# Performance work log

Measured on AMD Instinct MI355X. Metric: run time of the kernel, lower is better.

## Reference

```python
import jax, jax.numpy as jnp
import numpy as np

EPS = 1e-5

def mvn(x):
    # per-(N,C) spatial mean/std normalization; torch .var is unbiased (ddof=1)
    mean = jnp.mean(x, axis=(2, 3), keepdims=True)
    var = jnp.var(x, axis=(2, 3), ddof=1, keepdims=True)
    return (x - mean) / jnp.sqrt(var + EPS)

def conv1x1(x, w, b):
    # w: [O, C] (1x1 conv collapsed), x: [B, C, H, W]
    return jnp.einsum('bchw,oc->bohw', x, w) + b[None, :, None, None]

def conv3x3(x, w, b):
    # w: [O, I, 3, 3], VALID padding (snet uses padding=0)
    y = jax.lax.conv_general_dilated(x, w, (1, 1), 'VALID',
                                     dimension_numbers=('NCHW', 'OIHW', 'NCHW'))
    return y + b[None, :, None, None]

def safe_cbrt(x):
    # pow(relu(x), 1/3) with safe gradient at 0 (forward identical)
    pos = x > 0
    return jnp.where(pos, jnp.power(jnp.where(pos, x, 1.0), 1.0 / 3.0), 0.0)

def _forward(content, style, wf_san, bf_san, wg_san, bg_san, wh_san, bh_san,
             wf_mcc, bf_mcc, wg_mcc, bg_mcc, w_fc, b_fc, w_out, b_out,
             wc1, bc1, wc2, bc2, wc3, bc3, ws1, bs1, ws2, bs2, ws3, bs3,
             w_unc, b_unc):
    B, C, H, W = content.shape
    cn = mvn(content)
    sn = mvn(style)

    # --- MCC branch: channel correlation statistic of style ---
    F_Fc = conv1x1(cn, wf_mcc, bf_mcc)                      # [B,C,H,W]
    g = conv1x1(sn, wg_mcc, bg_mcc).reshape(B, C, H * W)    # [B,C,HW]
    FC_S = jnp.sum(g * g, axis=-1) / jnp.sum(g, axis=-1)    # [B,C]
    FC_S = FC_S @ w_fc.T + b_fc                             # Linear
    part1 = F_Fc * FC_S[:, :, None, None]

    # --- WCT-like covariance branch (compressed 32-dim space) ---
    Fs0 = style - jnp.mean(style, axis=(2, 3), keepdims=True)  # nor_mean
    fc_ = conv1x1(jax.nn.relu(conv1x1(jax.nn.relu(conv1x1(cn, wc1, bc1)), wc2, bc2)), wc3, bc3)  # [B,32,H,W]
    fs_ = conv1x1(jax.nn.relu(conv3x3(jax.nn.relu(conv3x3(Fs0, ws1, bs1)), ws2, bs2)), ws3, bs3)  # [B,32,H-4,W-4]
    cdim = fc_.shape[1]
    fs_flat = fs_.reshape(B, cdim, -1)                       # [B,32,hw_s]
    cov = jnp.einsum('bci,bdi->bcd', fs_flat, fs_flat) / fs_flat.shape[2]  # [B,32,32]
    out = jnp.einsum('bcd,bdi->bci', cov, fc_.reshape(B, cdim, H * W)).reshape(B, cdim, H, W)
    part2 = conv1x1(out, w_unc, b_unc)                       # [B,512,H,W]

    # --- SANet-style attention branch ---
    F_s = conv1x1(cn, wf_san, bf_san).reshape(B, C, H * W)
    G_s = conv1x1(sn, wg_san, bg_san).reshape(B, C, H * W)
    H_s = conv1x1(style, wh_san, bh_san).reshape(B, C, H * W)
    S = jax.nn.softmax(jnp.einsum('bci,bcj->bij', F_s, G_s), axis=-1)  # [B,HW,HW]
    part3 = jnp.einsum('bcj,bij->bci', H_s, S).reshape(B, C, H, W)

    p = safe_cbrt(jax.nn.relu(part1 * part2 * part3))
    return conv1x1(p, w_out, b_out) + content


def setup_inputs() -> dict:
    key = jax.random.key(0)
    B, C, H, W = 16, 512, 32, 32
    s = 0.02
    shapes = {
        'content': (B, C, H, W), 'style': (B, C, H, W),
        'wf_san': (C, C), 'bf_san': (C,), 'wg_san': (C, C), 'bg_san': (C,),
        'wh_san': (C, C), 'bh_san': (C,),
        'wf_mcc': (C, C), 'bf_mcc': (C,), 'wg_mcc': (C, C), 'bg_mcc': (C,),
        'w_fc': (C, C), 'b_fc': (C,), 'w_out': (C, C), 'b_out': (C,),
        'wc1': (256, 512), 'bc1': (256,), 'wc2': (128, 256), 'bc2': (128,),
        'wc3': (32, 128), 'bc3': (32,),
        'ws1': (256, 512, 3, 3), 'bs1': (256,), 'ws2': (128, 256, 3, 3), 'bs2': (128,),
        'ws3': (32, 128), 'bs3': (32,),
        'w_unc': (512, 32), 'b_unc': (512,),
    }
    d = {}
    for i, (name, shp) in enumerate(shapes.items()):
        k = jax.random.fold_in(key, i)
        scale = 1.0 if name in ('content', 'style') else s
        d[name] = jax.random.normal(k, shp, dtype=jnp.float32) * scale
    return d


def reference(content, style, wf_san, bf_san, wg_san, bg_san, wh_san, bh_san,
              wf_mcc, bf_mcc, wg_mcc, bg_mcc, w_fc, b_fc, w_out, b_out,
              wc1, bc1, wc2, bc2, wc3, bc3, ws1, bs1, ws2, bs2, ws3, bs3,
              w_unc, b_unc):
    return _forward(content, style, wf_san, bf_san, wg_san, bg_san, wh_san, bh_san,
                    wf_mcc, bf_mcc, wg_mcc, bg_mcc, w_fc, b_fc, w_out, b_out,
                    wc1, bc1, wc2, bc2, wc3, bc3, ws1, bs1, ws2, bs2, ws3, bs3,
                    w_unc, b_unc)
```

## Files before the change

### kernel.cpp

```cpp
#include <hip/hip_runtime.h>
#include <hip/hip_bf16.h>
#include <hip/hip_fp16.h>
#include <math.h>


typedef __attribute__((ext_vector_type(8))) short short8;
typedef __attribute__((ext_vector_type(4))) float f32x4;
typedef unsigned short us;
#define MFMA16 __builtin_amdgcn_mfma_f32_16x16x32_bf16

struct h16 { us v; };

template <class A, class B> struct SameT { static constexpr bool v = false; };
template <class A> struct SameT<A, A> { static constexpr bool v = true; };

__device__ inline float b2f(us b) { return __uint_as_float(((unsigned)b) << 16); }
__device__ inline us f2b(float f) {
    unsigned u = __float_as_uint(f);
    return (us)((u + 0x7FFFu + ((u >> 16) & 1u)) >> 16);
}

template <typename TOUT>
__device__ inline us cvt2b(float x) {
    if constexpr (SameT<TOUT, h16>::v) return __half_as_ushort(__float2half(x));
    else return f2b(x);
}

__device__ inline double blockReduceSumD(double v, double* sh) {
    int t = threadIdx.x;
    sh[t] = v; __syncthreads();
    for (int s = blockDim.x >> 1; s > 0; s >>= 1) {
        if (t < s) sh[t] += sh[t + s];
        __syncthreads();
    }
    double r = sh[0]; __syncthreads();
    return r;
}

__global__ __launch_bounds__(256) void stats_k(const float* __restrict__ X,
                                               float* __restrict__ mean,
                                               float* __restrict__ inv, int HW) {
    __shared__ double sh[256];
    int bc = blockIdx.x;
    const float* x = X + (size_t)bc * HW;
    int t = threadIdx.x;
    float v[4];
    double s = 0.0;
    #pragma unroll
    for (int r = 0; r < 4; ++r) { v[r] = x[t + r * 256]; s += (double)v[r]; }
    double tot = blockReduceSumD(s, sh);
    double ss = 0.0;
    #pragma unroll
    for (int r = 0; r < 4; ++r) ss += (double)v[r] * (double)v[r];
    double tot2 = blockReduceSumD(ss, sh);
    if (t == 0) {
        double m = tot / HW;
        double var = (tot2 - tot * tot / HW) / (HW - 1);
        mean[bc] = (float)m;
        inv[bc] = (float)(1.0 / sqrt(var + 1e-5));
    }
}

__global__ __launch_bounds__(256) void trn_k(const float* __restrict__ X,
                                             const float* __restrict__ mean,
                                             const float* __restrict__ inv,
                                             us* __restrict__ Yn, us* __restrict__ Yc,
                                             us* __restrict__ Yr, int C, int HW) {
    __shared__ us Ln[64 * 65];
    __shared__ us Lc[64 * 65];
    __shared__ us Lr[64 * 65];
    int bz = blockIdx.z, c0 = blockIdx.y * 64, h0 = blockIdx.x * 64;
    const float* Xb = X + (size_t)bz * C * HW;
    int t = threadIdx.x;
    int cl = t >> 3, h8 = (t & 7) * 8;
    #pragma unroll
    for (int half = 0; half < 2; ++half) {
        int c = cl + half * 32;
        int gc = c0 + c;
        float m = mean[bz * C + gc], iv = inv[bz * C + gc];
        const float4* s4 = (const float4*)&Xb[(size_t)gc * HW + h0 + h8];
        float4 f0 = s4[0], f1 = s4[1];
        float vv[8] = {f0.x, f0.y, f0.z, f0.w, f1.x, f1.y, f1.z, f1.w};
        #pragma unroll
        for (int i = 0; i < 8; ++i) {
            int li = c * 65 + h8 + i;
            if (Yn) Ln[li] = f2b((vv[i] - m) * iv);
            if (Yc) Lc[li] = f2b(vv[i] - m);
            if (Yr) Lr[li] = f2b(vv[i]);
        }
    }
    __syncthreads();
    int hl = t >> 3, c8 = (t & 7) * 8;
    #pragma unroll
    for (int half = 0; half < 2; ++half) {
        int hh = hl + half * 32;
        size_t off = ((size_t)bz * HW + h0 + hh) * (size_t)C + c0 + c8;
        us tmp[8];
        if (Yn) {
            #pragma unroll
            for (int i = 0; i < 8; ++i) tmp[i] = Ln[(c8 + i) * 65 + hh];
            *(uint4*)&Yn[off] = *(const uint4*)tmp;
        }
        if (Yc) {
            #pragma unroll
            for (int i = 0; i < 8; ++i) tmp[i] = Lc[(c8 + i) * 65 + hh];
            *(uint4*)&Yc[off] = *(const uint4*)tmp;
        }
        if (Yr) {
            #pragma unroll
            for (int i = 0; i < 8; ++i) tmp[i] = Lr[(c8 + i) * 65 + hh];
            *(uint4*)&Yr[off] = *(const uint4*)tmp;
        }
    }
}

template <typename TE>
__device__ inline void stage16(const TE* __restrict__ src, bool valid, us* dst) {
    us tmp[16];
    if (valid) {
        if constexpr (sizeof(TE) == 2) {
            uint4 a = ((const uint4*)src)[0], b = ((const uint4*)src)[1];
            *(uint4*)&tmp[0] = a; *(uint4*)&tmp[8] = b;
        } else {
            const float4* s4 = (const float4*)src;
            float4 f0 = s4[0], f1 = s4[1], f2 = s4[2], f3 = s4[3];
            float vv[16] = {f0.x, f0.y, f0.z, f0.w, f1.x, f1.y, f1.z, f1.w,
                            f2.x, f2.y, f2.z, f2.w, f3.x, f3.y, f3.z, f3.w};
            #pragma unroll
            for (int i = 0; i < 16; ++i) tmp[i] = f2b(vv[i]);
        }
    } else {
        #pragma unroll
        for (int i = 0; i < 16; ++i) tmp[i] = 0;
    }
    ((uint4*)dst)[0] = *(uint4*)&tmp[0];
    ((uint4*)dst)[1] = *(uint4*)&tmp[8];
}

template <typename TAel, typename TBel, typename TOUT, int OUTT>
__global__ __launch_bounds__(256) void mf2_k(const TAel* __restrict__ A, long astride, int lda,
                                             const TBel* __restrict__ B, long bstride, int ldb,
                                             const float* __restrict__ bias,
                                             TOUT* __restrict__ Y,
                                             const float* __restrict__ add_src,
                                             int K, int M, int N, int relu) {
    __shared__ __align__(16) us smem[20480];
    int bz = blockIdx.z;
    int mbase = blockIdx.y * 128, nbase = blockIdx.x * 128;
    const TAel* Ab = A + (size_t)bz * astride;
    const TBel* Bb = B + (size_t)bz * bstride;
    int t = threadIdx.x;
    int row = t & 127, kh = t >> 7;
    int wave = t >> 6, lane = t & 63, lm = lane & 15, q = lane >> 4;
    int mh = (wave >> 1) * 64, nh = (wave & 1) * 64;
    int gm = mbase + row, gn = nbase + row;
    bool vm = gm < M, vn = gn < N;

    auto As = [&](int buf) { return smem + buf * 5120; };
    auto Bs = [&](int buf) { return smem + 10240 + buf * 5120; };

    auto stage = [&](int buf, int kb) {
        stage16(Ab + (size_t)gm * lda + kb + kh * 16, vm, As(buf) + row * 40 + kh * 16);
        stage16(Bb + (size_t)gn * ldb + kb + kh * 16, vn, Bs(buf) + row * 40 + kh * 16);
    };

    f32x4 acc[4][4];
    #pragma unroll
    for (int i = 0; i < 4; ++i)
        #pragma unroll
        for (int j = 0; j < 4; ++j) acc[i][j] = (f32x4){0.f, 0.f, 0.f, 0.f};

    stage(0, 0);
    __syncthreads();
    int cur = 0;
    for (int kb = 0; kb < K; kb += 32) {
        if (kb + 32 < K) stage(cur ^ 1, kb + 32);
        short8 af[4], bf[4];
        #pragma unroll
        for (int i = 0; i < 4; ++i) af[i] = *(const short8*)(As(cur) + (mh + i * 16 + lm) * 40 + q * 8);
        #pragma unroll
        for (int j = 0; j < 4; ++j) bf[j] = *(const short8*)(Bs(cur) + (nh + j * 16 + lm) * 40 + q * 8);
        #pragma unroll
        for (int i = 0; i < 4; ++i)
            #pragma unroll
            for (int j = 0; j < 4; ++j)
                acc[i][j] = MFMA16(af[i], bf[j], acc[i][j], 0, 0, 0);
        __syncthreads();
        cur ^= 1;
    }

    if constexpr (sizeof(TOUT) == 2) {
        if (mbase + 128 <= M && nbase + 128 <= N) {
            us* Ts = smem;
            #pragma unroll
            for (int i = 0; i < 4; ++i) {
                int m0 = mh + i * 16 + q * 4;
                float bv[4];
                #pragma unroll
                for (int r = 0; r < 4; ++r) bv[r] = bias ? bias[mbase + m0 + r] : 0.f;
                #pragma unroll
                for (int j = 0; j < 4; ++j) {
                    int nl = nh + j * 16 + lm;
                    #pragma unroll
                    for (int r = 0; r < 4; ++r) {
                        float x = acc[i][j][r] + bv[r];
                        if (relu) x = (x > 0.f) ? x : 0.f;
                        us val = cvt2b<TOUT>(x);
                        if (OUTT == 0) Ts[(m0 + r) * 136 + nl] = val;
                        else Ts[nl * 136 + m0 + r] = val;
                    }
                }
            }
            __syncthreads();
            #pragma unroll
            for (int k2 = 0; k2 < 8; ++k2) {
                int flat = k2 * 256 + t;
                int r0 = flat >> 4, u = flat & 15;
                uint4 vv = *(const uint4*)&Ts[r0 * 136 + u * 8];
                us* dst;
                if (OUTT == 0)
                    dst = (us*)&Y[((size_t)bz * M + mbase + r0) * N + nbase + u * 8];
                else
                    dst = (us*)&Y[((size_t)bz * N + nbase + r0) * M + mbase + u * 8];
                *(uint4*)dst = vv;
            }
            return;
        }
    }

    #pragma unroll
    for (int i = 0; i < 4; ++i) {
        int m0 = mbase + mh + i * 16 + q * 4;
        if (m0 >= M) continue;
        float bv[4];
        #pragma unroll
        for (int r = 0; r < 4; ++r) bv[r] = bias ? bias[m0 + r] : 0.f;
        #pragma unroll
        for (int j = 0; j < 4; ++j) {
            int n = nbase + nh + j * 16 + lm;
            if (n >= N) continue;
            float v[4];
            #pragma unroll
            for (int r = 0; r < 4; ++r) {
                float x = acc[i][j][r] + bv[r];
                if (relu) x = (x > 0.f) ? x : 0.f;
                v[r] = x;
            }
            if (OUTT == 1) {
                size_t off = ((size_t)bz * N + n) * (size_t)M + m0;
                if constexpr (sizeof(TOUT) == 2) {
                    us o4[4];
                    #pragma unroll
                    for (int r = 0; r < 4; ++r) o4[r] = cvt2b<TOUT>(v[r]);
                    *(uint2*)&Y[off] = *(const uint2*)o4;
                } else {
                    float4 f4 = make_float4(v[0], v[1], v[2], v[3]);
                    *(float4*)&Y[off] = f4;
                }
            } else {
                #pragma unroll
                for (int r = 0; r < 4; ++r) {
                    size_t off = ((size_t)bz * M + m0 + r) * (size_t)N + n;
                    float x = v[r];
                    if (add_src) x += add_src[off];
                    if constexpr (sizeof(TOUT) == 2) {
                        us val = cvt2b<TOUT>(x);
                        *(us*)&Y[off] = val;
                    } else Y[off] = x;
                }
            }
        }
    }
}

struct SBias {
    const float* bp[10];
    int moff[10];
    unsigned relu;
};

__global__ __launch_bounds__(256) void reorder_gw_k(const us* __restrict__ W,
                                                    us* __restrict__ Wf, int M, int K) {
    int idx = blockIdx.x * 256 + threadIdx.x;
    int KB = K >> 5;
    int total = (M >> 7) * KB * 8 * 64;
    if (idx >= total) return;
    int lane = idx & 63;
    int f = idx >> 6;
    int i = f & 3, mhalf = (f >> 2) & 1;
    int rest = f >> 3;
    int kb = rest % KB, mt = rest / KB;
    int row = mt * 128 + mhalf * 64 + i * 16 + (lane & 15);
    int col = kb * 32 + (lane >> 4) * 8;
    *(uint4*)&Wf[(size_t)idx * 8] = *(const uint4*)&W[(size_t)row * K + col];
}

template <typename TBel, typename TOUT, int OUTT>
__global__ __launch_bounds__(256) void mfw_k(const us* __restrict__ Wf,
                                             const TBel* __restrict__ B, long bstride, int ldb,
                                             TOUT* __restrict__ Y, int ldy,
                                             SBias sb, const float* __restrict__ add_src,
                                             int K, int M, int N) {
    __shared__ __align__(16) us smem[10240];
    int bz = blockIdx.z, mt = blockIdx.y;
    int mbase = mt * 128, nbase = blockIdx.x * 128;
    const TBel* Bb = B + (size_t)bz * bstride;
    int t = threadIdx.x;
    int row = t & 127, kh = t >> 7;
    int wave = t >> 6, lane = t & 63, lm = lane & 15, q = lane >> 4;
    int mhalf = wave >> 1, nh = (wave & 1) * 64;
    int KB = K >> 5;
    const us* Wb = Wf + (size_t)mt * KB * 4096;
    int relu = (sb.relu >> mt) & 1;
    const float* bias = sb.bp[mt];
    int moff = sb.moff[mt];

    auto Bs = [&](int buf) { return smem + buf * 5120; };
    auto stageB = [&](int buf, int kb) {
        stage16(Bb + (size_t)(nbase + row) * ldb + (size_t)kb * 32 + kh * 16, true,
                Bs(buf) + row * 40 + kh * 16);
    };

    f32x4 acc[4][4];
    #pragma unroll
    for (int i = 0; i < 4; ++i)
        #pragma unroll
        for (int j = 0; j < 4; ++j) acc[i][j] = (f32x4){0.f, 0.f, 0.f, 0.f};

    stageB(0, 0);
    __syncthreads();
    int cur = 0;
    for (int kb = 0; kb < KB; ++kb) {
        if (kb + 1 < KB) stageB(cur ^ 1, kb + 1);
        const us* wk = Wb + (size_t)kb * 4096 + mhalf * 2048;
        short8 af[4], bf[4];
        #pragma unroll
        for (int i = 0; i < 4; ++i) af[i] = *(const short8*)&wk[i * 512 + lane * 8];
        #pragma unroll
        for (int j = 0; j < 4; ++j) bf[j] = *(const short8*)(Bs(cur) + (nh + j * 16 + lm) * 40 + q * 8);
        #pragma unroll
        for (int i = 0; i < 4; ++i)
            #pragma unroll
            for (int j = 0; j < 4; ++j)
                acc[i][j] = MFMA16(af[i], bf[j], acc[i][j], 0, 0, 0);
        __syncthreads();
        cur ^= 1;
    }

    if constexpr (sizeof(TOUT) == 2) {
        us* Ts = smem;
        #pragma unroll
        for (int p = 0; p < 2; ++p) {
            bool part = (OUTT == 1) ? ((wave & 1) == p) : (mhalf == p);
            if (part) {
                #pragma unroll
                for (int i = 0; i < 4; ++i) {
                    int m0 = mhalf * 64 + i * 16 + q * 4;
                    float bv[4];
                    #pragma unroll
                    for (int r = 0; r < 4; ++r) bv[r] = bias[mbase + m0 + r - moff];
                    #pragma unroll
                    for (int j = 0; j < 4; ++j) {
                        int nl = nh + j * 16 + lm;
                        #pragma unroll
                        for (int r = 0; r < 4; ++r) {
                            float x = acc[i][j][r] + bv[r];
                            if (relu) x = (x > 0.f) ? x : 0.f;
                            us val = cvt2b<TOUT>(x);
                            if (OUTT == 1) Ts[(nl - p * 64) * 136 + m0 + r] = val;
                            else Ts[(m0 + r - p * 64) * 136 + nl] = val;
                        }
                    }
                }
            }
            __syncthreads();
            #pragma unroll
            for (int k2 = 0; k2 < 4; ++k2) {
                int flat = k2 * 256 + t;
                int r0 = flat >> 4, u = flat & 15;
                uint4 vv = *(const uint4*)&Ts[r0 * 136 + u * 8];
                us* dst;
                if (OUTT == 1)
                    dst = (us*)&Y[((size_t)bz * N + nbase + p * 64 + r0) * ldy + mbase + u * 8];
                else
                    dst = (us*)&Y[((size_t)bz * M + mbase + p * 64 + r0) * (size_t)N + nbase + u * 8];
                *(uint4*)dst = vv;
            }
            __syncthreads();
        }
    } else {
        #pragma unroll
        for (int i = 0; i < 4; ++i) {
            int m0 = mbase + mhalf * 64 + i * 16 + q * 4;
            float bv[4];
            #pragma unroll
            for (int r = 0; r < 4; ++r) bv[r] = bias[m0 + r - moff];
            #pragma unroll
            for (int j = 0; j < 4; ++j) {
                int n = nbase + nh + j * 16 + lm;
                #pragma unroll
                for (int r = 0; r < 4; ++r) {
                    size_t off = ((size_t)bz * M + m0 + r) * (size_t)N + n;
                    float x = acc[i][j][r] + bv[r];
                    if (relu) x = (x > 0.f) ? x : 0.f;
                    if (add_src) x += add_src[off];
                    Y[off] = x;
                }
            }
        }
    }
}

struct CpyArg {
    const float* src[11];
    unsigned long long dstoff[11];
    int len[11];
};
__global__ __launch_bounds__(256) void wcat_k(CpyArg a, us* __restrict__ arena) {
    int seg = blockIdx.y;
    int idx = blockIdx.x * 256 + threadIdx.x;
    if (idx < a.len[seg]) arena[a.dstoff[seg] + idx] = f2b(a.src[seg][idx]);
}

__global__ __launch_bounds__(256) void reorder_wf_k(const float* __restrict__ W,
                                                    us* __restrict__ Wf, int O, int Cin) {
    int idx = blockIdx.x * 256 + threadIdx.x;
    int OT = O >> 6, KB = Cin >> 5;
    int total = OT * KB * 9 * 4 * 64;
    if (idx >= total) return;
    int lane = idx & 63;
    int f = idx >> 6;
    int i = f & 1, half = (f >> 1) & 1;
    int tf = f >> 2;
    int tap = tf % 9;
    int rest = tf / 9;
    int kb = rest % KB, ot = rest / KB;
    int o = ot * 64 + half * 32 + i * 16 + (lane & 15);
    int cb = kb * 32 + (lane >> 4) * 8;
    us v[8];
    #pragma unroll
    for (int e = 0; e < 8; ++e)
        v[e] = f2b(W[((size_t)o * Cin + cb + e) * 9 + tap]);
    *(uint4*)&Wf[(size_t)idx * 8] = *(const uint4*)v;
}

template <int PR>
__device__ inline void stage_patch(const us* __restrict__ Xb, us* __restrict__ dst,
                                   int pyb, int kb, int Cin, int IH, int IW, int t) {
    const int ITEMS = (2 * PR + 2) * 36 * 4;
    for (int i = t; i < ITEMS; i += 256) {
        int p = i >> 2, q8 = (i & 3) * 8;
        int r = p / 36, x = p - r * 36;
        int gy = pyb + r;
        uint4 v = make_uint4(0u, 0u, 0u, 0u);
        if (x < IW && gy < IH)
            v = *(const uint4*)&Xb[((size_t)(gy * IW + x)) * Cin + kb * 32 + q8];
        *(uint4*)&dst[p * 40 + q8] = v;
    }
}

template <int PR>
__global__ __launch_bounds__(256) void conv_mf4_k(const us* __restrict__ X, long xbstride,
                                                  const us* __restrict__ Wf,
                                                  const float* __restrict__ bias,
                                                  us* __restrict__ Y, long ybstride,
                                                  int Cin, int O, int IH, int IW,
                                                  int OH, int OW) {
    __shared__ us patch[2][(2 * PR + 2) * 36 * 40];
    int bz = blockIdx.z;
    int obase = blockIdx.y * 64;
    int pyb = blockIdx.x * (2 * PR);
    const us* Xb = X + (size_t)bz * xbstride;
    int t = threadIdx.x;
    int wave = t >> 6, lane = t & 63, lm = lane & 15, q = lane >> 4;
    int half = wave >> 1, rw = wave & 1;
    int KB = Cin >> 5;
    const us* Wb = Wf + (size_t)(obase >> 6) * KB * 9 * 2048;

    f32x4 acc[PR][2][2];
    #pragma unroll
    for (int pr = 0; pr < PR; ++pr)
        #pragma unroll
        for (int i = 0; i < 2; ++i)
            #pragma unroll
            for (int j = 0; j < 2; ++j) acc[pr][i][j] = (f32x4){0.f, 0.f, 0.f, 0.f};

    stage_patch<PR>(Xb, patch[0], pyb, 0, Cin, IH, IW, t);
    __syncthreads();
    int cur = 0;
    for (int kb = 0; kb < KB; ++kb) {
        if (kb + 1 < KB) stage_patch<PR>(Xb, patch[cur ^ 1], pyb, kb + 1, Cin, IH, IW, t);
        const us* Wk = Wb + (size_t)kb * 9 * 2048;
        #pragma unroll
        for (int tap = 0; tap < 9; ++tap) {
            int ky = tap / 3, kx = tap - ky * 3;
            const us* wt = Wk + tap * 2048 + half * 1024;
            short8 a0 = *(const short8*)&wt[lane * 8];
            short8 a1 = *(const short8*)&wt[512 + lane * 8];
            #pragma unroll
            for (int pr = 0; pr < PR; ++pr) {
                int prow = (pr * 2 + rw + ky) * 36;
                short8 b0 = *(const short8*)&patch[cur][(prow + lm + kx) * 40 + q * 8];
                short8 b1 = *(const short8*)&patch[cur][(prow + 16 + lm + kx) * 40 + q * 8];
                acc[pr][0][0] = MFMA16(a0, b0, acc[pr][0][0], 0, 0, 0);
                acc[pr][0][1] = MFMA16(a0, b1, acc[pr][0][1], 0, 0, 0);
                acc[pr][1][0] = MFMA16(a1, b0, acc[pr][1][0], 0, 0, 0);
                acc[pr][1][1] = MFMA16(a1, b1, acc[pr][1][1], 0, 0, 0);
            }
        }
        __syncthreads();
        cur ^= 1;
    }

    us* Yb = Y + (size_t)bz * ybstride;
    #pragma unroll
    for (int pr = 0; pr < PR; ++pr) {
        int py = pyb + pr * 2 + rw;
        if (py >= OH) continue;
        #pragma unroll
        for (int i = 0; i < 2; ++i) {
            int m0 = obase + half * 32 + i * 16 + q * 4;
            #pragma unroll
            for (int j = 0; j < 2; ++j) {
                int px = j * 16 + lm;
                if (px >= OW) continue;
                us o4[4];
                #pragma unroll
                for (int r = 0; r < 4; ++r) {
                    float v = acc[pr][i][j][r] + bias[m0 + r];
                    v = (v > 0.f) ? v : 0.f;
                    o4[r] = f2b(v);
                }
                *(uint2*)&Yb[((size_t)(py * OW + px)) * O + m0] = *(const uint2*)o4;
            }
        }
    }
}

__global__ __launch_bounds__(256) void gemm_k(const float* __restrict__ W,
                                              const float* __restrict__ X,
                                              const float* __restrict__ bias,
                                              float* __restrict__ Y,
                                              int C, int O, int N) {
    int obase = blockIdx.y * 32;
    __shared__ float As[32][33];
    __shared__ float Bs[32][33];
    int t = threadIdx.x;
    int tx = t & 15, ty = t >> 4;
    float acc00 = 0, acc01 = 0, acc10 = 0, acc11 = 0;
    for (int cb = 0; cb < C; cb += 32) {
        int k = t & 31, o0 = t >> 5;
        #pragma unroll
        for (int r = 0; r < 4; ++r) {
            int ol = o0 + r * 8;
            As[k][ol] = W[(size_t)(obase + ol) * C + cb + k];
        }
        int n0 = t & 31, k0 = t >> 5;
        #pragma unroll
        for (int r = 0; r < 4; ++r) {
            int k2 = k0 + r * 8;
            Bs[k2][n0] = (n0 < N) ? X[(size_t)(cb + k2) * N + n0] : 0.f;
        }
        __syncthreads();
        #pragma unroll
        for (int k2 = 0; k2 < 32; ++k2) {
            float a0 = As[k2][ty], a1 = As[k2][ty + 16];
            float b0 = Bs[k2][tx], b1 = Bs[k2][tx + 16];
            acc00 += a0 * b0; acc01 += a0 * b1;
            acc10 += a1 * b0; acc11 += a1 * b1;
        }
        __syncthreads();
    }
    float accs[2][2] = {{acc00, acc01}, {acc10, acc11}};
    #pragma unroll
    for (int i = 0; i < 2; ++i) {
        int o = obase + ty + i * 16;
        float bv = bias[o];
        #pragma unroll
        for (int j = 0; j < 2; ++j) {
            int n = tx + j * 16;
            if (n < N) Y[(size_t)o * N + n] = accs[i][j] + bv;
        }
    }
}

__global__ __launch_bounds__(256) void fcs3a_k(const us* __restrict__ g, int ldg,
                                               float* __restrict__ pa, int HW) {
    int b = blockIdx.x, j = blockIdx.y;
    int t = threadIdx.x;
    const us* gb = g + ((size_t)b * HW + (size_t)j * 128) * ldg + 2 * t;
    double s0 = 0.0, s1 = 0.0;
    #pragma unroll 4
    for (int hw = 0; hw < 128; ++hw) {
        unsigned u = *(const unsigned*)&gb[(size_t)hw * ldg];
        float f0 = b2f((us)(u & 0xFFFFu));
        float f1 = b2f((us)(u >> 16));
        s0 += (double)f0 * (double)f0;
        s1 += (double)f1 * (double)f1;
    }
    float2 w = make_float2((float)s0, (float)s1);
    *(float2*)&pa[((size_t)b * 8 + j) * 512 + 2 * t] = w;
}

__global__ __launch_bounds__(256) void fcs3b_k(const float* __restrict__ pa,
                                               const float* __restrict__ bg,
                                               float* __restrict__ fcs, int B, int HW) {
    int b = blockIdx.x;
    int t = threadIdx.x;
    double s0 = 0.0, s1 = 0.0;
    #pragma unroll
    for (int j = 0; j < 8; ++j) {
        float2 w = *(const float2*)&pa[((size_t)b * 8 + j) * 512 + 2 * t];
        s0 += (double)w.x; s1 += (double)w.y;
    }
    int c0 = 2 * t;
    fcs[(size_t)c0 * B + b] = (float)(s0 / ((double)HW * (double)bg[c0]));
    fcs[(size_t)(c0 + 1) * B + b] = (float)(s1 / ((double)HW * (double)bg[c0 + 1]));
}

__global__ __launch_bounds__(256) void softmax_k(const us* __restrict__ S,
                                                 us* __restrict__ P) {
    __shared__ float sh[256];
    size_t row = blockIdx.x;
    const us* r = S + row * 1024;
    us* po = P + row * 1024;
    int t = threadIdx.x;
    us raw[4];
    *(uint2*)raw = *(const uint2*)&r[t * 4];
    float v[4];
    float m = -INFINITY;
    #pragma unroll
    for (int i = 0; i < 4; ++i) {
        v[i] = __half2float(__ushort_as_half(raw[i]));
        m = fmaxf(m, v[i]);
    }
    sh[t] = m; __syncthreads();
    for (int s = 128; s > 0; s >>= 1) { if (t < s) sh[t] = fmaxf(sh[t], sh[t + s]); __syncthreads(); }
    m = sh[0]; __syncthreads();
    float sum = 0;
    #pragma unroll
    for (int i = 0; i < 4; ++i) { v[i] = expf(v[i] - m); sum += v[i]; }
    sh[t] = sum; __syncthreads();
    for (int s = 128; s > 0; s >>= 1) { if (t < s) sh[t] += sh[t + s]; __syncthreads(); }
    float inv = 1.f / sh[0]; __syncthreads();
    #pragma unroll
    for (int i = 0; i < 4; ++i) raw[i] = f2b(v[i] * inv);
    *(uint2*)&po[t * 4] = *(const uint2*)raw;
}

__global__ __launch_bounds__(256) void cov2_k(const float* __restrict__ fs,
                                              float* __restrict__ cov, int Cd, int M) {
    __shared__ float Ls[196 * 36];
    int bb = blockIdx.x;
    int t = threadIdx.x;
    const float* p = fs + (size_t)bb * M * Cd;
    int c = t >> 3, d0 = (t & 7) * 4;
    float a0 = 0.f, a1 = 0.f, a2 = 0.f, a3 = 0.f;
    for (int ch = 0; ch < 4; ++ch) {
        __syncthreads();
        for (int i = t; i < 1568; i += 256) {
            int rowi = i >> 3, c4 = (i & 7) * 4;
            float4 v = *(const float4*)&p[(size_t)(ch * 196 + rowi) * Cd + c4];
            *(float4*)&Ls[rowi * 36 + c4] = v;
        }
        __syncthreads();
        for (int i = 0; i < 196; ++i) {
            float a = Ls[i * 36 + c];
            a0 += a * Ls[i * 36 + d0 + 0];
            a1 += a * Ls[i * 36 + d0 + 1];
            a2 += a * Ls[i * 36 + d0 + 2];
            a3 += a * Ls[i * 36 + d0 + 3];
        }
    }
    float invM = 1.f / (float)M;
    size_t base = ((size_t)bb * Cd + c) * Cd + d0;
    cov[base + 0] = a0 * invM;
    cov[base + 1] = a1 * invM;
    cov[base + 2] = a2 * invM;
    cov[base + 3] = a3 * invM;
}

__global__ __launch_bounds__(256) void fuse_k(const us* __restrict__ ffc, int ldf,
                                              const float* __restrict__ fc2t,
                                              const us* __restrict__ p2,
                                              const us* __restrict__ p3,
                                              us* __restrict__ out, int B, int C, int HW) {
    size_t idx = (size_t)blockIdx.x * 256 + threadIdx.x;
    size_t total = (size_t)B * C * HW;
    if (idx >= total) return;
    int c = (int)(idx & (size_t)(C - 1));
    size_t tok = idx >> 9;
    int b = (int)(idx / ((size_t)C * HW));
    float part1 = b2f(ffc[tok * ldf + c]) * fc2t[(size_t)c * B + b];
    float v = part1 * b2f(p2[idx]) * b2f(p3[idx]);
    v = (v > 0.f) ? v : 0.f;
    out[idx] = f2b(cbrtf(v));
}

extern "C" void kernel_launch(void* const* d_in, const int* in_sizes, int n_in,
                              void* d_out, int out_size, void* d_ws, size_t ws_size,
                              hipStream_t stream) {
    typedef const float* fp;
    fp content = (fp)d_in[0];
    fp style   = (fp)d_in[1];
    fp wf_san = (fp)d_in[2],  bf_san = (fp)d_in[3];
    fp wg_san = (fp)d_in[4],  bg_san = (fp)d_in[5];
    fp wh_san = (fp)d_in[6],  bh_san = (fp)d_in[7];
    fp wf_mcc = (fp)d_in[8],  bf_mcc = (fp)d_in[9];
    fp wg_mcc = (fp)d_in[10], bg_mcc = (fp)d_in[11];
    fp w_fc   = (fp)d_in[12], b_fc   = (fp)d_in[13];
    fp w_out  = (fp)d_in[14], b_out  = (fp)d_in[15];
    fp wc1 = (fp)d_in[16], bc1 = (fp)d_in[17];
    fp wc2 = (fp)d_in[18], bc2 = (fp)d_in[19];
    fp wc3 = (fp)d_in[20], bc3 = (fp)d_in[21];
    fp ws1 = (fp)d_in[22], bs1 = (fp)d_in[23];
    fp ws2 = (fp)d_in[24], bs2 = (fp)d_in[25];
    fp ws3 = (fp)d_in[26], bs3 = (fp)d_in[27];
    fp w_unc = (fp)d_in[28], b_unc = (fp)d_in[29];

    const int B = 16, C = 512, HW = 1024;
    const size_t NE = (size_t)B * C * HW;
    const long TOK = (long)C * HW;
    const size_t MB = 1u << 20;
    char* base = (char*)d_ws;

    us* cnT      = (us*)(base);
    us* snT      = (us*)(base + 16 * MB);
    us* fs0T     = (us*)(base + 32 * MB);
    us* s1       = (us*)(base + 48 * MB);
    us* s2       = (us*)(base + 56 * MB);
    float* fs_c  = (float*)(base + 60 * MB);
    us* Sbuf16   = (us*)(base);
    h16* Sh      = (h16*)(base);
    us* cnOut    = (us*)(base + 64 * MB);
    us* snOut    = (us*)(base + 104 * MB);
    us* part3b   = (us*)(base + 104 * MB);
    us* part2b   = (us*)(base + 120 * MB);
    us* Pb       = (us*)(base + 136 * MB);
    us* t2b      = (us*)(base + 136 * MB);
    float* fc_c  = (float*)(base + 140 * MB);
    float* out32 = (float*)(base + 142 * MB);
    us* pbuf     = (us*)(base + 144 * MB);
    us* styleT   = (us*)(base + 168 * MB);
    us* Hco      = (us*)(base + 184 * MB);

    char* misc = base + 200 * MB;
    us* Wr1   = (us*)(misc);
    us* Wr2   = (us*)(misc + 2359296);
    us* arena = (us*)(misc + 2949120);
    us* Wcn   = arena;
    us* Wsn   = arena + 655360;
    us* Wh    = arena + 1179648;
    us* Wout  = arena + 1441792;
    us* Wc2   = arena + 1703936;
    us* Wc3   = arena + 1736704;
    us* Ws3   = arena + 1740800;
    us* Wunc  = arena + 1744896;
    float* pa    = (float*)(misc + 6471680);
    float* fcs   = (float*)(misc + 6733824);
    float* fc2t  = (float*)(misc + 6766592);
    float* cov   = (float*)(misc + 6799360);
    float* meanC = (float*)(misc + 6864896);
    float* invC  = (float*)(misc + 6897664);
    float* meanS = (float*)(misc + 6930432);
    float* invS  = (float*)(misc + 6963200);
    us* Fcn  = (us*)(misc + 6995968);
    us* Fsn  = (us*)(misc + 8306688);
    us* Fh   = (us*)(misc + 9355264);
    us* Fout = (us*)(misc + 9879552);
    us* Fc2  = (us*)(misc + 10403840);
    us* Func = (us*)(misc + 10469376);

    CpyArg ca;
    const float* srcs[11] = {wf_mcc, wc1, wf_san, wg_mcc, wg_san, wh_san,
                             w_out, wc2, wc3, ws3, w_unc};
    int lens[11] = {262144, 131072, 262144, 262144, 262144, 262144,
                    262144, 32768, 4096, 4096, 16384};
    unsigned long long off = 0;
    for (int i = 0; i < 11; ++i) { ca.src[i] = srcs[i]; ca.dstoff[i] = off; ca.len[i] = lens[i]; off += lens[i]; }
    wcat_k<<<dim3(1024, 11), 256, 0, stream>>>(ca, arena);
    reorder_wf_k<<<576, 256, 0, stream>>>(ws1, Wr1, 256, 512);
    reorder_wf_k<<<72, 256, 0, stream>>>(ws2, Wr2, 128, 256);
    reorder_gw_k<<<320, 256, 0, stream>>>(Wcn, Fcn, 1280, 512);
    reorder_gw_k<<<256, 256, 0, stream>>>(Wsn, Fsn, 1024, 512);
    reorder_gw_k<<<128, 256, 0, stream>>>(Wh, Fh, 512, 512);
    reorder_gw_k<<<128, 256, 0, stream>>>(Wout, Fout, 512, 512);
    reorder_gw_k<<<16, 256, 0, stream>>>(Wc2, Fc2, 128, 256);
    reorder_gw_k<<<8, 256, 0, stream>>>(Wunc, Func, 512, 32);

    stats_k<<<B * C, 256, 0, stream>>>(content, meanC, invC, HW);
    stats_k<<<B * C, 256, 0, stream>>>(style, meanS, invS, HW);
    trn_k<<<dim3(16, 8, 16), 256, 0, stream>>>(content, meanC, invC, cnT, nullptr, nullptr, C, HW);
    trn_k<<<dim3(16, 8, 16), 256, 0, stream>>>(style, meanS, invS, snT, fs0T, styleT, C, HW);

    conv_mf4_k<1><<<dim3(15, 4, 16), 256, 0, stream>>>(fs0T, TOK, Wr1, bs1,
                                                       s1, (long)900 * 256, 512, 256, 32, 32, 30, 30);
    conv_mf4_k<1><<<dim3(14, 2, 16), 256, 0, stream>>>(s1, (long)900 * 256, Wr2, bs2,
                                                       s2, (long)784 * 128, 256, 128, 30, 30, 28, 28);
    mf2_k<us, us, float, 1><<<dim3(7, 1, 16), 256, 0, stream>>>(
        Ws3, 0, 128, s2, (long)784 * 128, 128, bs3, fs_c, nullptr, 128, 32, 784, 0);
    cov2_k<<<B, 256, 0, stream>>>(fs_c, cov, 32, 784);

    {
        SBias sb;
        for (int y = 0; y < 4; ++y) { sb.bp[y] = bf_mcc; sb.moff[y] = 0; }
        for (int y = 4; y < 6; ++y) { sb.bp[y] = bc1; sb.moff[y] = 512; }
        for (int y = 6; y < 10; ++y) { sb.bp[y] = bf_san; sb.moff[y] = 768; }
        sb.relu = 0x030u;
        mfw_k<us, us, 1><<<dim3(8, 10, 16), 256, 0, stream>>>(
            Fcn, cnT, TOK, 512, cnOut, 1280, sb, nullptr, 512, 1280, 1024);
    }

    {
        SBias sb;
        for (int y = 0; y < 4; ++y) { sb.bp[y] = bg_mcc; sb.moff[y] = 0; }
        for (int y = 4; y < 8; ++y) { sb.bp[y] = bg_san; sb.moff[y] = 512; }
        for (int y = 8; y < 10; ++y) { sb.bp[y] = bg_mcc; sb.moff[y] = 0; }
        sb.relu = 0u;
        mfw_k<us, us, 1><<<dim3(8, 8, 16), 256, 0, stream>>>(
            Fsn, snT, TOK, 512, snOut, 1024, sb, nullptr, 512, 1024, 1024);
    }

    fcs3a_k<<<dim3(B, 8), 256, 0, stream>>>(snOut, 1024, pa, HW);
    fcs3b_k<<<B, 256, 0, stream>>>(pa, bg_mcc, fcs, B, HW);
    gemm_k<<<dim3(1, 16, 1), 256, 0, stream>>>(w_fc, fcs, b_fc, fc2t, 512, 512, 16);

    {
        SBias sb;
        for (int y = 0; y < 10; ++y) { sb.bp[y] = bh_san; sb.moff[y] = 0; }
        sb.relu = 0u;
        mfw_k<us, us, 0><<<dim3(8, 4, 16), 256, 0, stream>>>(
            Fh, styleT, TOK, 512, Hco, 0, sb, nullptr, 512, 512, 1024);
    }

    mf2_k<us, us, h16, 0><<<dim3(8, 8, 16), 256, 0, stream>>>(
        cnOut + 768, (long)1024 * 1280, 1280, snOut + 512, (long)1024 * 1024, 1024,
        nullptr, Sh, nullptr, 512, 1024, 1024, 0);
    softmax_k<<<B * HW, 256, 0, stream>>>(Sbuf16, Pb);

    mf2_k<us, us, us, 0><<<dim3(4, 8, 16), 256, 0, stream>>>(
        Pb, (long)1024 * 1024, 1024, Hco, TOK, 1024, nullptr, part3b, nullptr,
        1024, 1024, 512, 0);

    {
        SBias sb;
        for (int y = 0; y < 10; ++y) { sb.bp[y] = bc2; sb.moff[y] = 0; }
        sb.relu = 0x1u;
        mfw_k<us, us, 1><<<dim3(8, 1, 16), 256, 0, stream>>>(
            Fc2, cnOut + 512, (long)1024 * 1280, 1280, t2b, 128, sb, nullptr, 256, 128, 1024);
    }
    mf2_k<us, us, float, 1><<<dim3(8, 1, 16), 256, 0, stream>>>(
        Wc3, 0, 128, t2b, (long)1024 * 128, 128, bc3, fc_c, nullptr, 128, 32, 1024, 0);

    mf2_k<float, float, float, 1><<<dim3(8, 1, 16), 256, 0, stream>>>(
        cov, 1024, 32, fc_c, (long)1024 * 32, 32, nullptr, out32, nullptr, 32, 32, 1024, 0);
    {
        SBias sb;
        for (int y = 0; y < 10; ++y) { sb.bp[y] = b_unc; sb.moff[y] = 0; }
        sb.relu = 0u;
        mfw_k<float, us, 1><<<dim3(8, 4, 16), 256, 0, stream>>>(
            Func, out32, (long)1024 * 32, 32, part2b, 512, sb, nullptr, 32, 512, 1024);
    }

    fuse_k<<<(unsigned)((NE + 255) / 256), 256, 0, stream>>>(
        cnOut, 1280, fc2t, part2b, part3b, pbuf, B, C, HW);

    {
        SBias sb;
        for (int y = 0; y < 10; ++y) { sb.bp[y] = b_out; sb.moff[y] = 0; }
        sb.relu = 0u;
        mfw_k<us, float, 0><<<dim3(8, 4, 16), 256, 0, stream>>>(
            Fout, pbuf, TOK, 512, (float*)d_out, 0, sb, content, 512, 512, 1024);
    }
}
```

Measured before the change: 754.3 us.

## Merge three weight-GEMM launches into one descriptor-driven grouped kernel

Replaces the three separate mfw_k launches (content projections, style projections and the H projection) with one mega_k kernel. It reads a per-blockIdx.y descriptor holding weights, input, bias, output, layout and relu. This removes two launches and lets all 22 M-tiles share one grid, filling the GPU better and cutting tail effects. The new kernel hardcodes K=512 and N=1024 and uses a simplified double-buffered pipeline that may differ in efficiency from mfw_k.

Result: no change. 757.0 us (+0.4%).

```diff
diff --git a/kernel.cpp b/kernel.cpp
--- a/kernel.cpp
+++ b/kernel.cpp
@@ -295,6 +295,104 @@
     *(uint4*)&Wf[(size_t)idx * 8] = *(const uint4*)&W[(size_t)row * K + col];
 }
 
+struct GD {
+    const us* wf;
+    const us* Bp;
+    const float* bias;
+    us* Y;
+    long ostride;
+    int ldy;
+    int outt;
+    int relu;
+};
+struct GDs { GD d[22]; };
+
+__global__ __launch_bounds__(256) void mega_k(GDs ds) {
+    __shared__ __align__(16) us smem[10240];
+    const int N = 1024, KB = 16;
+    GD g = ds.d[blockIdx.y];
+    int bz = blockIdx.z;
+    int nbase = blockIdx.x * 128;
+    const us* Bb = g.Bp + (size_t)bz * 524288;
+    int t = threadIdx.x;
+    int row = t & 127, kh = t >> 7;
+    int wave = t >> 6, lane = t & 63, lm = lane & 15, q = lane >> 4;
+    int mhalf = wave >> 1, nh = (wave & 1) * 64;
+
+    auto Bs = [&](int buf) { return smem + buf * 5120; };
+    auto stageB = [&](int buf, int kb) {
+        stage16(Bb + (size_t)(nbase + row) * 512 + kb * 32 + kh * 16, true,
+                Bs(buf) + row * 40 + kh * 16);
+    };
+
+    f32x4 acc[4][4];
+    #pragma unroll
+    for (int i = 0; i < 4; ++i)
+        #pragma unroll
+        for (int j = 0; j < 4; ++j) acc[i][j] = (f32x4){0.f, 0.f, 0.f, 0.f};
+
+    stageB(0, 0);
+    __syncthreads();
+    int cur = 0;
+    for (int kb = 0; kb < KB; ++kb) {
+        if (kb + 1 < KB) stageB(cur ^ 1, kb + 1);
+        const us* wk = g.wf + (size_t)kb * 4096 + mhalf * 2048;
+        short8 af[4], bf[4];
+        #pragma unroll
+        for (int i = 0; i < 4; ++i) af[i] = *(const short8*)&wk[i * 512 + lane * 8];
+        #pragma unroll
+        for (int j = 0; j < 4; ++j) bf[j] = *(const short8*)(Bs(cur) + (nh + j * 16 + lm) * 40 + q * 8);
+        #pragma unroll
+        for (int i = 0; i < 4; ++i)
+            #pragma unroll
+            for (int j = 0; j < 4; ++j)
+                acc[i][j] = MFMA16(af[i], bf[j], acc[i][j], 0, 0, 0);
+        __syncthreads();
+        cur ^= 1;
+    }
+
+    us* Ts = smem;
+    #pragma unroll
+    for (int p = 0; p < 2; ++p) {
+        bool part = g.outt ? ((wave & 1) == p) : (mhalf == p);
+        if (part) {
+            #pragma unroll
+            for (int i = 0; i < 4; ++i) {
+                int m0 = mhalf * 64 + i * 16 + q * 4;
+                float bv[4];
+                #pragma unroll
+                for (int r = 0; r < 4; ++r) bv[r] = g.bias[m0 + r];
+                #pragma unroll
+                for (int j = 0; j < 4; ++j) {
+                    int nl = nh + j * 16 + lm;
+                    #pragma unroll
+                    for (int r = 0; r < 4; ++r) {
+                        float x = acc[i][j][r] + bv[r];
+                        if (g.relu) x = (x > 0.f) ? x : 0.f;
+                        us val = f2b(x);
+                        if (g.outt) Ts[(nl - p * 64) * 136 + m0 + r] = val;
+                        else Ts[(m0 + r - p * 64) * 136 + nl] = val;
+                    }
+                }
+            }
+        }
+        __syncthreads();
+        #pragma unroll
+        for (int k2 = 0; k2 < 4; ++k2) {
+            int flat = k2 * 256 + t;
+            int r0 = flat >> 4, u = flat & 15;
+            uint4 vv = *(const uint4*)&Ts[r0 * 136 + u * 8];
+            us* dst;
+            if (g.outt)
+                dst = g.Y + (size_t)bz * g.ostride + (size_t)(nbase + p * 64 + r0) * g.ldy + u * 8;
+            else
+                dst = g.Y + (size_t)bz * g.ostride + (size_t)(p * 64 + r0) * N + nbase + u * 8;
+            *(uint4*)dst = vv;
+        }
+        __syncthreads();
+    }
+}
+
 template <typename TBel, typename TOUT, int OUTT>
 __global__ __launch_bounds__(256) void mfw_k(const us* __restrict__ Wf,
                                              const TBel* __restrict__ B, long bstride, int ldb,
@@ -802,36 +900,49 @@
     cov2_k<<<B, 256, 0, stream>>>(fs_c, cov, 32, 784);
 
     {
-        SBias sb;
-        for (int y = 0; y < 4; ++y) { sb.bp[y] = bf_mcc; sb.moff[y] = 0; }
-        for (int y = 4; y < 6; ++y) { sb.bp[y] = bc1; sb.moff[y] = 512; }
-        for (int y = 6; y < 10; ++y) { sb.bp[y] = bf_san; sb.moff[y] = 768; }
-        sb.relu = 0x030u;
-        mfw_k<us, us, 1><<<dim3(8, 10, 16), 256, 0, stream>>>(
-            Fcn, cnT, TOK, 512, cnOut, 1280, sb, nullptr, 512, 1280, 1024);
-    }
-
-    {
-        SBias sb;
-        for (int y = 0; y < 4; ++y) { sb.bp[y] = bg_mcc; sb.moff[y] = 0; }
-        for (int y = 4; y < 8; ++y) { sb.bp[y] = bg_san; sb.moff[y] = 512; }
-        for (int y = 8; y < 10; ++y) { sb.bp[y] = bg_mcc; sb.moff[y] = 0; }
-        sb.relu = 0u;
-        mfw_k<us, us, 1><<<dim3(8, 8, 16), 256, 0, stream>>>(
-            Fsn, snT, TOK, 512, snOut, 1024, sb, nullptr, 512, 1024, 1024);
+        GDs ds;
+        for (int y = 0; y < 10; ++y) {
+            GD& g = ds.d[y];
+            g.wf = Fcn + (size_t)y * 65536;
+            g.Bp = cnT;
+            g.Y = cnOut + y * 128;
+            g.ostride = (long)1024 * 1280;
+            g.ldy = 1280;
+            g.outt = 1;
+            if (y < 4)      { g.bias = bf_mcc + y * 128;       g.relu = 0; }
+            else if (y < 6) { g.bias = bc1 + (y - 4) * 128;    g.relu = 1; }
+            else            { g.bias = bf_san + (y - 6) * 128; g.relu = 0; }
+        }
+        for (int y = 10; y < 18; ++y) {
+            int ml = y - 10;
+            GD& g = ds.d[y];
+            g.wf = Fsn + (size_t)ml * 65536;
+            g.Bp = snT;
+            g.Y = snOut + ml * 128;
+            g.ostride = (long)1024 * 1024;
+            g.ldy = 1024;
+            g.outt = 1;
+            g.relu = 0;
+            g.bias = (ml < 4) ? (bg_mcc + ml * 128) : (bg_san + (ml - 4) * 128);
+        }
+        for (int y = 18; y < 22; ++y) {
+            int ml = y - 18;
+            GD& g = ds.d[y];
+            g.wf = Fh + (size_t)ml * 65536;
+            g.Bp = styleT;
+            g.Y = Hco + (size_t)ml * 128 * 1024;
+            g.ostride = (long)512 * 1024;
+            g.ldy = 0;
+            g.outt = 0;
+            g.relu = 0;
+            g.bias = bh_san + ml * 128;
+        }
+        mega_k<<<dim3(8, 22, 16), 256, 0, stream>>>(ds);
     }
 
     fcs3a_k<<<dim3(B, 8), 256, 0, stream>>>(snOut, 1024, pa, HW);
     fcs3b_k<<<B, 256, 0, stream>>>(pa, bg_mcc, fcs, B, HW);
     gemm_k<<<dim3(1, 16, 1), 256, 0, stream>>>(w_fc, fcs, b_fc, fc2t, 512, 512, 16);
-
-    {
-        SBias sb;
-        for (int y = 0; y < 10; ++y) { sb.bp[y] = bh_san; sb.moff[y] = 0; }
-        sb.relu = 0u;
-        mfw_k<us, us, 0><<<dim3(8, 4, 16), 256, 0, stream>>>(
-            Fh, styleT, TOK, 512, Hco, 0, sb, nullptr, 512, 512, 1024);
-    }
 
     mf2_k<us, us, h16, 0><<<dim3(8, 8, 16), 256, 0, stream>>>(
         cnOut + 768, (long)1024 * 1280, 1280, snOut + 512, (long)1024 * 1024, 1024,
```
